# Performance work log

Measured on AMD Instinct MI355X. Metric: run time of the kernel, lower is better.

The kernel has to match this reference:

```python
import jax, jax.numpy as jnp
import numpy as np

N = 16000        # nodes
E = 256000       # edges
D_IN = 1280      # input node features
HID = 256        # hidden dim (all hidden_dims equal; required by res_linear shapes)
HEADS = 8
C = HID // HEADS # 32 channels per head
G = 32           # graphs in the batch
O = 64           # output labels (GO terms)
NB = 2           # conv blocks = len(hidden_dims) - 1
EPS = 1e-5


def _bn(h, g, b):
    # eval-mode BatchNorm1d with running_mean=0, running_var=1 (init state)
    return h * (g / jnp.sqrt(1.0 + EPS)) + b


def _seg_softmax(logits, seg, num):
    # numerically-stable segment softmax (PyG softmax semantics)
    m = jax.ops.segment_max(logits, seg, num_segments=num)
    e = jnp.exp(logits - m[seg])
    s = jax.ops.segment_sum(e, seg, num_segments=num)
    return e / (s[seg] + 1e-16)


def setup_inputs() -> dict:
    key = jax.random.key(0)
    ks = jax.random.split(key, 16)
    w = lambda i, sh: jax.random.normal(ks[i], sh, jnp.float32) * 0.05
    return {
        "x": jax.random.normal(ks[0], (N, D_IN), jnp.float32),
        "edge_index": jax.random.randint(ks[1], (2, E), 0, N),
        "batch": jnp.sort(jax.random.randint(ks[2], (N,), 0, G)),
        # feature_proj: Linear -> ReLU -> BN
        "fp_W": w(3, (D_IN, HID)), "fp_b": jnp.zeros(HID),
        "fp_g": jnp.ones(HID), "fp_be": jnp.zeros(HID),
        # GATv2Conv per block: lin_l, lin_r, att, out-bias
        "gat_Wl": w(4, (NB, HID, HID)), "gat_bl": jnp.zeros((NB, HID)),
        "gat_Wr": w(5, (NB, HID, HID)), "gat_br": jnp.zeros((NB, HID)),
        "gat_att": w(6, (NB, HEADS, C)), "gat_bias": jnp.zeros((NB, HID)),
        # GINConv MLP: Linear -> ReLU -> BN
        "gin_W": w(7, (NB, HID, HID)), "gin_b": jnp.zeros((NB, HID)),
        "gin_g": jnp.ones((NB, HID)), "gin_be": jnp.zeros((NB, HID)),
        # PyG LayerNorm (graph mode) affine
        "ln_g": jnp.ones((NB, HID)), "ln_b": jnp.zeros((NB, HID)),
        # residual linears
        "res_W": w(8, (NB, HID, HID)), "res_b": jnp.zeros((NB, HID)),
        # GlobalAttention gate MLP
        "pool_W1": w(9, (HID, HID)), "pool_b1": jnp.zeros(HID),
        "pool_W2": w(10, (HID, 1)), "pool_b2": jnp.zeros(1),
        # O label heads (hierarchy=None -> just the MLP), stacked
        "head_W1": w(11, (O, HID, 256)), "head_b1": jnp.zeros((O, 256)),
        "head_g": jnp.ones((O, 256)), "head_be": jnp.zeros((O, 256)),
        "head_W2": w(12, (O, 256)), "head_b2": jnp.zeros(O),
    }


def reference(x, edge_index, batch, fp_W, fp_b, fp_g, fp_be,
              gat_Wl, gat_bl, gat_Wr, gat_br, gat_att, gat_bias,
              gin_W, gin_b, gin_g, gin_be, ln_g, ln_b, res_W, res_b,
              pool_W1, pool_b1, pool_W2, pool_b2,
              head_W1, head_b1, head_g, head_be, head_W2, head_b2):
    n = x.shape[0]
    # feature_proj (eval: dropout = identity)
    h = _bn(jax.nn.relu(x @ fp_W + fp_b), fp_g, fp_be)

    src0, dst0 = edge_index[0], edge_index[1]
    loop = jnp.arange(n)
    src = jnp.concatenate([src0, loop])  # GATv2 adds self-loops by default
    dst = jnp.concatenate([dst0, loop])

    for i in range(NB):
        # ---- GATv2Conv (no activation after, per original control flow) ----
        xl = (h @ gat_Wl[i] + gat_bl[i]).reshape(n, HEADS, C)
        xr = (h @ gat_Wr[i] + gat_br[i]).reshape(n, HEADS, C)
        msg = xl[src]                                   # [E', H, C]
        eact = jax.nn.leaky_relu(msg + xr[dst], 0.2)
        logit = jnp.einsum('ehc,hc->eh', eact, gat_att[i])
        alpha = _seg_softmax(logit, dst, n)             # [E', H]
        h = jax.ops.segment_sum(alpha[:, :, None] * msg, dst,
                                num_segments=n).reshape(n, HID) + gat_bias[i]
        # ---- GINConv: nn((1+0)*x + sum_neighbors), then leaky_relu ----
        agg = jax.ops.segment_sum(h[src0], dst0, num_segments=n)
        gin = _bn(jax.nn.relu((h + agg) @ gin_W[i] + gin_b[i]), gin_g[i], gin_be[i])
        h = jax.nn.leaky_relu(gin, 0.2)
        # ---- PyG LayerNorm (graph mode, batch=None: global mean/std) + residual ----
        mu = h.mean()
        sd = jnp.std(h)
        ln = (h - mu) / (sd + EPS) * ln_g[i] + ln_b[i]
        h = jax.nn.leaky_relu(ln + (h @ res_W[i] + res_b[i]), 0.2)

    # ---- GlobalAttention pooling ----
    gate = jnp.tanh(h @ pool_W1 + pool_b1) @ pool_W2 + pool_b2   # [N, 1]
    a = _seg_softmax(gate[:, 0], batch, G)
    emb = jax.ops.segment_sum(a[:, None] * h, batch, num_segments=G)  # [G, HID]

    # ---- O label heads (hierarchy None -> MLP only), vectorized ----
    z = jnp.einsum('bd,odh->boh', emb, head_W1) + head_b1[None]
    z = _bn(jax.nn.silu(z), head_g[None], head_be[None])
    out = jnp.einsum('boh,oh->bo', z, head_W2) + head_b2[None]
    return out[:, :, None]  # torch.stack(outputs, dim=1) -> [G, O, 1]
```

## Files before the change

kernel.cpp:

```cpp
#include <hip/hip_runtime.h>
#include <math.h>

#define N_NODES 16000
#define N_EDGES 256000
#define EPE (N_EDGES + N_NODES)
#define DIN 1280
#define HID 256
#define HEADS 8
#define CPH 32
#define NG 32
#define NO 64
#define EPSC 1e-5f
#define CAP 32
#define XPAD 264

typedef __bf16 bf16;
typedef __attribute__((ext_vector_type(8))) __bf16 bf16x8;
typedef __attribute__((ext_vector_type(4))) float floatx4;

typedef __attribute__((address_space(3))) unsigned int lds_u32;
typedef const __attribute__((address_space(1))) unsigned int glob_u32;

__device__ __forceinline__ float lrelu(float v) { return v > 0.f ? v : 0.2f * v; }
__device__ __forceinline__ float bflo(unsigned int u) { return __uint_as_float(u << 16); }
__device__ __forceinline__ float bfhi(unsigned int u) { return __uint_as_float(u & 0xffff0000u); }

__device__ __forceinline__ void gll16(const void* g, void* l) {
    __builtin_amdgcn_global_load_lds((glob_u32*)g, (lds_u32*)l, 16, 0, 0);
}

__global__ void wconv_gen(const float* __restrict__ W, bf16* __restrict__ Wt, int K, int total) {
    int idx = blockIdx.x * 256 + threadIdx.x;
    if (idx >= total) return;
    int per = K * HID;
    int l = idx / per, rem = idx - l * per;
    int n = rem / K, k = rem - n * K;
    Wt[idx] = (bf16)W[(size_t)l * per + (size_t)k * HID + n];
}

__global__ void wconv_pair(const float* __restrict__ Wl, const float* __restrict__ Wr,
                           bf16* __restrict__ Wt) {
    int idx = blockIdx.x * 256 + threadIdx.x;
    int n = idx >> 8, k = idx & 255;
    float v = (n < 256) ? Wl[(size_t)k * HID + n] : Wr[(size_t)k * HID + (n - 256)];
    Wt[idx] = (bf16)v;
}

__global__ __launch_bounds__(256) void gemm_mfma(
    const bf16* __restrict__ A, const bf16* __restrict__ Bt,
    const float* __restrict__ bias, const float* __restrict__ bias2,
    bf16* __restrict__ C, int K, int ldc, int mode,
    const float* __restrict__ g, const float* __restrict__ be)
{
    __shared__ __align__(16) bf16 As[128 * 32];
    __shared__ __align__(16) bf16 Bs[128 * 32];
    const int tid = threadIdx.x;
    const int bm = blockIdx.y * 128, bn = blockIdx.x * 128;
    const int w = tid >> 6, lane = tid & 63;
    const int wm = (w & 1) * 64, wn = (w >> 1) * 64;
    const int lrow = lane & 15, lk8 = (lane >> 4) * 8;

    floatx4 acc[4][4];
#pragma unroll
    for (int i = 0; i < 4; i++)
#pragma unroll
        for (int j = 0; j < 4; j++) acc[i][j] = (floatx4){0.f, 0.f, 0.f, 0.f};

    const bf16* gA = A + (size_t)(bm + (tid >> 2)) * K + (tid & 3) * 8;
    const bf16* gB = Bt + (size_t)(bn + (tid >> 2)) * K + (tid & 3) * 8;
    bf16* lA0 = As + (size_t)(w * 64) * 8;
    bf16* lA1 = As + (size_t)(w * 64 + 256) * 8;
    bf16* lB0 = Bs + (size_t)(w * 64) * 8;
    bf16* lB1 = Bs + (size_t)(w * 64 + 256) * 8;
    const size_t rowskip = (size_t)64 * K;

    for (int k0 = 0; k0 < K; k0 += 32) {
        gll16(gA + k0, lA0);
        gll16(gA + rowskip + k0, lA1);
        gll16(gB + k0, lB0);
        gll16(gB + rowskip + k0, lB1);
        __syncthreads();
        bf16x8 af[4], bfr[4];
#pragma unroll
        for (int i = 0; i < 4; i++) af[i] = *(const bf16x8*)&As[(wm + 16 * i + lrow) * 32 + lk8];
#pragma unroll
        for (int j = 0; j < 4; j++) bfr[j] = *(const bf16x8*)&Bs[(wn + 16 * j + lrow) * 32 + lk8];
#pragma unroll
        for (int i = 0; i < 4; i++)
#pragma unroll
            for (int j = 0; j < 4; j++)
                acc[i][j] = __builtin_amdgcn_mfma_f32_16x16x32_bf16(af[i], bfr[j], acc[i][j], 0, 0, 0);
        __syncthreads();
    }

    const float inv = rsqrtf(1.f + EPSC);
#pragma unroll
    for (int j = 0; j < 4; j++) {
        int col = bn + wn + 16 * j + lrow;
        float bcol = (col < HID) ? bias[col] : bias2[col - HID];
        float gc = (mode >= 1) ? g[col] * inv : 0.f;
        float bec = (mode >= 1) ? be[col] : 0.f;
#pragma unroll
        for (int i = 0; i < 4; i++) {
            int row0 = bm + wm + 16 * i + (lane >> 4) * 4;
#pragma unroll
            for (int r = 0; r < 4; r++) {
                float z = acc[i][j][r] + bcol;
                if (mode >= 1) { z = fmaxf(z, 0.f); z = z * gc + bec; }
                if (mode == 2) z = lrelu(z);
                C[(size_t)(row0 + r) * ldc + col] = (bf16)z;
            }
        }
    }
}

__global__ __launch_bounds__(256) void gemm_f32A(
    const float* __restrict__ A, const bf16* __restrict__ Bt,
    const float* __restrict__ bias, bf16* __restrict__ C, int K,
    const float* __restrict__ g, const float* __restrict__ be)
{
    __shared__ __align__(16) bf16 As[128 * 32];
    __shared__ __align__(16) bf16 Bs[128 * 32];
    const int tid = threadIdx.x;
    const int bm = blockIdx.y * 128, bn = blockIdx.x * 128;
    const int w = tid >> 6, lane = tid & 63;
    const int wm = (w & 1) * 64, wn = (w >> 1) * 64;
    const int lrow = lane & 15, lk8 = (lane >> 4) * 8;

    floatx4 acc[4][4];
#pragma unroll
    for (int i = 0; i < 4; i++)
#pragma unroll
        for (int j = 0; j < 4; j++) acc[i][j] = (floatx4){0.f, 0.f, 0.f, 0.f};

    const int r2 = tid >> 1, c2 = tid & 1;
    const float* gA = A + (size_t)(bm + r2) * K + c2 * 16;
    bf16* sA = As + r2 * 32 + c2 * 16;
    const bf16* gB = Bt + (size_t)(bn + (tid >> 2)) * K + (tid & 3) * 8;
    bf16* lB0 = Bs + (size_t)(w * 64) * 8;
    bf16* lB1 = Bs + (size_t)(w * 64 + 256) * 8;
    const size_t rowskipB = (size_t)64 * K;

    for (int k0 = 0; k0 < K; k0 += 32) {
        gll16(gB + k0, lB0);
        gll16(gB + rowskipB + k0, lB1);
        float4 a0 = *(const float4*)(gA + k0 + 0);
        float4 a1 = *(const float4*)(gA + k0 + 4);
        float4 a2 = *(const float4*)(gA + k0 + 8);
        float4 a3 = *(const float4*)(gA + k0 + 12);
        bf16x8 h0, h1;
        h0[0] = (bf16)a0.x; h0[1] = (bf16)a0.y; h0[2] = (bf16)a0.z; h0[3] = (bf16)a0.w;
        h0[4] = (bf16)a1.x; h0[5] = (bf16)a1.y; h0[6] = (bf16)a1.z; h0[7] = (bf16)a1.w;
        h1[0] = (bf16)a2.x; h1[1] = (bf16)a2.y; h1[2] = (bf16)a2.z; h1[3] = (bf16)a2.w;
        h1[4] = (bf16)a3.x; h1[5] = (bf16)a3.y; h1[6] = (bf16)a3.z; h1[7] = (bf16)a3.w;
        *(bf16x8*)(sA + 0) = h0;
        *(bf16x8*)(sA + 8) = h1;
        __syncthreads();
        bf16x8 af[4], bfr[4];
#pragma unroll
        for (int i = 0; i < 4; i++) af[i] = *(const bf16x8*)&As[(wm + 16 * i + lrow) * 32 + lk8];
#pragma unroll
        for (int j = 0; j < 4; j++) bfr[j] = *(const bf16x8*)&Bs[(wn + 16 * j + lrow) * 32 + lk8];
#pragma unroll
        for (int i = 0; i < 4; i++)
#pragma unroll
            for (int j = 0; j < 4; j++)
                acc[i][j] = __builtin_amdgcn_mfma_f32_16x16x32_bf16(af[i], bfr[j], acc[i][j], 0, 0, 0);
        __syncthreads();
    }

    const float inv = rsqrtf(1.f + EPSC);
#pragma unroll
    for (int j = 0; j < 4; j++) {
        int col = bn + wn + 16 * j + lrow;
        float bcol = bias[col];
        float gc = g[col] * inv;
        float bec = be[col];
#pragma unroll
        for (int i = 0; i < 4; i++) {
            int row0 = bm + wm + 16 * i + (lane >> 4) * 4;
#pragma unroll
            for (int r = 0; r < 4; r++) {
                float z = fmaxf(acc[i][j][r] + bcol, 0.f) * gc + bec;
                C[(size_t)(row0 + r) * HID + col] = (bf16)z;
            }
        }
    }
}

__global__ void hist_kernel(const int* __restrict__ ei, int* __restrict__ cnt) {
    int e = blockIdx.x * 256 + threadIdx.x;
    if (e >= EPE) return;
    int d = (e < N_EDGES) ? ei[N_EDGES + e] : (e - N_EDGES);
    atomicAdd(&cnt[d], 1);
}

__global__ __launch_bounds__(1024) void scan_kernel(const int* __restrict__ cnt,
                                                    int* __restrict__ roff, int* __restrict__ cursor) {
    __shared__ int wsum[16];
    int t = threadIdx.x;
    int base = t * 16;
    int local[16]; int s = 0;
#pragma unroll
    for (int i = 0; i < 16; i++) {
        int idx = base + i;
        int v = (idx < N_NODES) ? cnt[idx] : 0;
        local[i] = s; s += v;
    }
    int lane = t & 63, wid = t >> 6;
    int incl = s;
    for (int o = 1; o < 64; o <<= 1) { int v = __shfl_up(incl, o); if (lane >= o) incl += v; }
    if (lane == 63) wsum[wid] = incl;
    __syncthreads();
    if (t == 0) { int a = 0; for (int k = 0; k < 16; k++) { int v = wsum[k]; wsum[k] = a; a += v; } }
    __syncthreads();
    int texcl = incl - s + wsum[wid];
#pragma unroll
    for (int i = 0; i < 16; i++) {
        int idx = base + i;
        if (idx < N_NODES) { int o = texcl + local[i]; roff[idx] = o; cursor[idx] = o; }
    }
    if (t == 1023) roff[N_NODES] = texcl + s;
}

__global__ void scatter_kernel(const int* __restrict__ ei, int* __restrict__ cursor,
                               int* __restrict__ esrc) {
    int e = blockIdx.x * 256 + threadIdx.x;
    if (e >= EPE) return;
    int s, d;
    if (e < N_EDGES) { s = ei[e]; d = ei[N_EDGES + e]; }
    else { s = d = e - N_EDGES; }
    int pos = atomicAdd(&cursor[d], 1);
    esrc[pos] = s;
}

__global__ __launch_bounds__(256) void gat_fused(
    const bf16* __restrict__ XLR, const int* __restrict__ roff, const int* __restrict__ esrc,
    const float* __restrict__ att, const float* __restrict__ gbias, bf16* __restrict__ out)
{
    const int d = blockIdx.x, t = threadIdx.x;
    const int beg = roff[d], deg = roff[d + 1] - beg;
    __shared__ __align__(16) bf16 xs[CAP][XPAD];
    __shared__ __align__(16) float4 xa4[8 * 16];
    __shared__ float llog[CAP * 8];
    __shared__ float m_s[8], s_s[8], resc[8];

    if (t < 128) {
        int hh = t >> 4, cc = t & 15;
        int c = hh * 32 + cc * 2;
        float xr0 = (float)XLR[(size_t)d * 512 + 256 + c];
        float xr1 = (float)XLR[(size_t)d * 512 + 256 + c + 1];
        xa4[hh * 16 + cc] = (float4){xr0, att[c], xr1, att[c + 1]};
    }
    if (t < 8) { m_s[t] = -INFINITY; s_s[t] = 0.f; }

    const int jj = t & 31;
    const int hh = t >> 5;
    const int g = t >> 5, l = t & 31;
    float acc = 0.f;

    for (int c0 = 0; c0 < deg; c0 += CAP) {
        int cn = min(CAP, deg - c0);
        __syncthreads();
        for (int r = g; r < cn; r += 8) {
            int s = esrc[beg + c0 + r];
            *(bf16x8*)(&xs[r][l * 8]) = *(const bf16x8*)(XLR + (size_t)s * 512 + l * 8);
        }
        __syncthreads();
        if (jj < cn) {
            float lg = 0.f;
#pragma unroll
            for (int cc = 0; cc < 16; cc++) {
                int ce = (cc + jj) & 15;
                unsigned int p = *(const unsigned int*)&xs[jj][hh * 32 + ce * 2];
                float4 xa = xa4[hh * 16 + ce];
                lg += lrelu(bflo(p) + xa.x) * xa.y + lrelu(bfhi(p) + xa.z) * xa.w;
            }
            llog[jj * 8 + hh] = lg;
        }
        __syncthreads();
        if (t < 64) {
            int h2 = t & 7, j0 = t >> 3;
            float mx = -INFINITY;
            for (int j = j0; j < cn; j += 8) mx = fmaxf(mx, llog[j * 8 + h2]);
            for (int o = 8; o < 64; o <<= 1) mx = fmaxf(mx, __shfl_xor(mx, o));
            float mo = m_s[h2];
            float mn = fmaxf(mo, mx);
            float ss = 0.f;
            for (int j = j0; j < cn; j += 8) {
                float e = __expf(llog[j * 8 + h2] - mn);
                llog[j * 8 + h2] = e;
                ss += e;
            }
            for (int o = 8; o < 64; o <<= 1) ss += __shfl_xor(ss, o);
            if (t < 8) {
                float r = __expf(mo - mn);
                resc[h2] = r;
                s_s[h2] = s_s[h2] * r + ss;
                m_s[h2] = mn;
            }
        }
        __syncthreads();
        acc *= resc[hh];
        for (int j = 0; j < cn; j++)
            acc += llog[j * 8 + hh] * (float)xs[j][t];
    }
    out[(size_t)d * HID + t] = (bf16)(gbias[t] + acc / (s_s[hh] + 1e-16f));
}

__global__ __launch_bounds__(256) void gin_gather(
    const unsigned int* __restrict__ hu, const int* __restrict__ roff,
    const int* __restrict__ esrc, unsigned int* __restrict__ uu)
{
    int d = blockIdx.x, t = threadIdx.x;
    int grp = t >> 7, c = t & 127;
    int beg = roff[d], end = roff[d + 1];
    float a0 = 0.f, a1 = 0.f;
    int p = beg + grp;
    while (p + 14 < end) {
        int s[8];
#pragma unroll
        for (int k = 0; k < 8; k++) s[k] = esrc[p + 2 * k];
        unsigned int v[8];
#pragma unroll
        for (int k = 0; k < 8; k++) v[k] = hu[(size_t)s[k] * 128 + c];
#pragma unroll
        for (int k = 0; k < 8; k++) { a0 += bflo(v[k]); a1 += bfhi(v[k]); }
        p += 16;
    }
    for (; p < end; p += 2) {
        unsigned int v = hu[(size_t)esrc[p] * 128 + c];
        a0 += bflo(v); a1 += bfhi(v);
    }
    __shared__ float plo[128], phi[128];
    if (grp) { plo[c] = a0; phi[c] = a1; }
    __syncthreads();
    if (!grp) {
        a0 += plo[c]; a1 += phi[c];
        bf16 b0 = (bf16)a0, b1 = (bf16)a1;
        unsigned int r = ((unsigned int)*(unsigned short*)&b0) |
                         (((unsigned int)*(unsigned short*)&b1) << 16);
        uu[(size_t)d * 128 + c] = r;
    }
}

__global__ void stats_kernel(const bf16* __restrict__ x, float2* __restrict__ part, int n8) {
    float s = 0.f, sq = 0.f;
    for (int i = blockIdx.x * blockDim.x + threadIdx.x; i < n8; i += gridDim.x * blockDim.x) {
        bf16x8 v = *(const bf16x8*)(x + (size_t)i * 8);
#pragma unroll
        for (int j = 0; j < 8; j++) { float f = (float)v[j]; s += f; sq += f * f; }
    }
    for (int o = 32; o > 0; o >>= 1) { s += __shfl_down(s, o); sq += __shfl_down(sq, o); }
    __shared__ float ls[4], lq[4];
    int wid = threadIdx.x >> 6, lane = threadIdx.x & 63;
    if (lane == 0) { ls[wid] = s; lq[wid] = sq; }
    __syncthreads();
    if (threadIdx.x == 0)
        part[blockIdx.x] = make_float2(ls[0] + ls[1] + ls[2] + ls[3],
                                       lq[0] + lq[1] + lq[2] + lq[3]);
}

__global__ void stats_reduce(const float2* __restrict__ part, float* __restrict__ stat) {
    int t = threadIdx.x;
    float2 v = part[t];
    float s = v.x, q = v.y;
    for (int o = 32; o > 0; o >>= 1) { s += __shfl_down(s, o); q += __shfl_down(q, o); }
    __shared__ float ls[4], lq[4];
    int wid = t >> 6, lane = t & 63;
    if (lane == 0) { ls[wid] = s; lq[wid] = q; }
    __syncthreads();
    if (t == 0) { stat[0] = ls[0] + ls[1] + ls[2] + ls[3]; stat[1] = lq[0] + lq[1] + lq[2] + lq[3]; }
}

__global__ void ln_res_kernel(const bf16* __restrict__ h, const bf16* __restrict__ r,
                              const float* __restrict__ stats, const float* __restrict__ g,
                              const float* __restrict__ b, bf16* __restrict__ out)
{
    int i = (blockIdx.x * 256 + threadIdx.x) * 4;
    const float inv_n = 1.f / (float)((size_t)N_NODES * HID);
    float mu = stats[0] * inv_n;
    float var = stats[1] * inv_n - mu * mu;
    float sd = sqrtf(fmaxf(var, 0.f));
    float rs = 1.f / (sd + EPSC);
    int ch = i & (HID - 1);
#pragma unroll
    for (int j = 0; j < 4; j++) {
        float v = ((float)h[i + j] - mu) * rs * g[ch + j] + b[ch + j] + (float)r[i + j];
        out[i + j] = (bf16)lrelu(v);
    }
}

__global__ void gbound_kernel(const int* __restrict__ batch, int* __restrict__ gstart) {
    int g = threadIdx.x;
    if (g > NG) return;
    int lo = 0, hi = N_NODES;
    while (lo < hi) { int mid = (lo + hi) >> 1; if (batch[mid] < g) lo = mid + 1; else hi = mid; }
    gstart[g] = lo;
}

__global__ __launch_bounds__(256) void pool_gate_kernel(const bf16* __restrict__ t,
    const float* __restrict__ W2, const float* __restrict__ b2, float* __restrict__ gate)
{
    int n = blockIdx.x * 4 + (threadIdx.x >> 6);
    int lane = threadIdx.x & 63;
    const bf16* p = t + (size_t)n * HID + lane * 4;
    float4 w = *(const float4*)(W2 + lane * 4);
    float s = tanhf((float)p[0]) * w.x + tanhf((float)p[1]) * w.y
            + tanhf((float)p[2]) * w.z + tanhf((float)p[3]) * w.w;
    for (int o = 32; o > 0; o >>= 1) s += __shfl_down(s, o);
    if (lane == 0) gate[n] = s + b2[0];
}

__global__ __launch_bounds__(256) void pool_stats_kernel(
    float* __restrict__ gate, const int* __restrict__ gstart)
{
    int g = blockIdx.x, t = threadIdx.x;
    int lo = gstart[g], hi = gstart[g + 1];
    __shared__ float red[256];
    float m = -INFINITY;
    for (int n = lo + t; n < hi; n += 256) m = fmaxf(m, gate[n]);
    red[t] = m; __syncthreads();
    for (int st = 128; st > 0; st >>= 1) { if (t < st) red[t] = fmaxf(red[t], red[t + st]); __syncthreads(); }
    m = red[0]; __syncthreads();
    float s = 0.f;
    for (int n = lo + t; n < hi; n += 256) s += __expf(gate[n] - m);
    red[t] = s; __syncthreads();
    for (int st = 128; st > 0; st >>= 1) { if (t < st) red[t] += red[t + st]; __syncthreads(); }
    float sinv = 1.f / (red[0] + 1e-16f);
    for (int n = lo + t; n < hi; n += 256) gate[n] = __expf(gate[n] - m) * sinv;
}

__global__ __launch_bounds__(256) void emb_accum_kernel(
    const float* __restrict__ a, const int* __restrict__ batch,
    const bf16* __restrict__ h, float* __restrict__ emb)
{
    int n0 = blockIdx.x * 32, t = threadIdx.x;
    int cur = batch[n0]; float acc = 0.f;
    for (int j = 0; j < 32; j++) {
        int n = n0 + j;
        int b = batch[n];
        if (b != cur) { atomicAdd(&emb[cur * HID + t], acc); cur = b; acc = 0.f; }
        acc += a[n] * (float)h[(size_t)n * HID + t];
    }
    atomicAdd(&emb[cur * HID + t], acc);
}

__global__ __launch_bounds__(256) void heads_kernel(
    const float* __restrict__ emb, const float* __restrict__ W1, const float* __restrict__ b1,
    const float* __restrict__ hg, const float* __restrict__ hbe, const float* __restrict__ W2,
    const float* __restrict__ b2, float* __restrict__ out)
{
    int o = blockIdx.x;
    int g0 = blockIdx.y * 4;
    int k = threadIdx.x;
    __shared__ float se[4][HID];
    __shared__ float red[256];
#pragma unroll
    for (int j = 0; j < 4; j++) se[j][k] = emb[(g0 + j) * HID + k];
    __syncthreads();
    const float* w1p = W1 + (size_t)o * HID * HID + k;
    float zb = b1[o * HID + k];
    float z0 = zb, z1 = zb, z2 = zb, z3 = zb;
#pragma unroll 8
    for (int d = 0; d < HID; d++) {
        float w = w1p[(size_t)d * HID];
        z0 = fmaf(se[0][d], w, z0);
        z1 = fmaf(se[1][d], w, z1);
        z2 = fmaf(se[2][d], w, z2);
        z3 = fmaf(se[3][d], w, z3);
    }
    const float gk = hg[o * HID + k] * rsqrtf(1.f + EPSC);
    const float bek = hbe[o * HID + k];
    const float w2 = W2[o * HID + k];
    const float b2o = b2[o];
    float zz[4] = {z0, z1, z2, z3};
#pragma unroll
    for (int j = 0; j < 4; j++) {
        float z = zz[j];
        float sil = z / (1.f + expf(-z));
        red[k] = (sil * gk + bek) * w2;
        __syncthreads();
        for (int st = 128; st > 0; st >>= 1) { if (k < st) red[k] += red[k + st]; __syncthreads(); }
        if (k == 0) out[(g0 + j) * NO + o] = red[0] + b2o;
        __syncthreads();
    }
}

extern "C" void kernel_launch(void* const* d_in, const int* in_sizes, int n_in,
                              void* d_out, int out_size, void* d_ws, size_t ws_size,
                              hipStream_t stream) {
    const float* x        = (const float*)d_in[0];
    const int*   ei       = (const int*)  d_in[1];
    const int*   batch    = (const int*)  d_in[2];
    const float* fp_W     = (const float*)d_in[3];
    const float* fp_b     = (const float*)d_in[4];
    const float* fp_g     = (const float*)d_in[5];
    const float* fp_be    = (const float*)d_in[6];
    const float* gat_Wl   = (const float*)d_in[7];
    const float* gat_bl   = (const float*)d_in[8];
    const float* gat_Wr   = (const float*)d_in[9];
    const float* gat_br   = (const float*)d_in[10];
    const float* gat_att  = (const float*)d_in[11];
    const float* gat_bias = (const float*)d_in[12];
    const float* gin_W    = (const float*)d_in[13];
    const float* gin_b    = (const float*)d_in[14];
    const float* gin_g    = (const float*)d_in[15];
    const float* gin_be   = (const float*)d_in[16];
    const float* ln_g     = (const float*)d_in[17];
    const float* ln_b     = (const float*)d_in[18];
    const float* res_W    = (const float*)d_in[19];
    const float* res_b    = (const float*)d_in[20];
    const float* pool_W1  = (const float*)d_in[21];
    const float* pool_b1  = (const float*)d_in[22];
    const float* pool_W2  = (const float*)d_in[23];
    const float* pool_b2  = (const float*)d_in[24];
    const float* head_W1  = (const float*)d_in[25];
    const float* head_b1  = (const float*)d_in[26];
    const float* head_g   = (const float*)d_in[27];
    const float* head_be  = (const float*)d_in[28];
    const float* head_W2  = (const float*)d_in[29];
    const float* head_b2  = (const float*)d_in[30];
    float* out = (float*)d_out;

    char* base = (char*)d_ws;
    size_t off = 0;
    auto alloc = [&](size_t bytes) -> char* {
        char* p = base + off; off += (bytes + 255) & ~(size_t)255; return p;
    };
    int*   esrc   = (int*)  alloc((size_t)EPE * 4);
    int*   cnt    = (int*)  alloc((size_t)N_NODES * 4);
    int*   roff   = (int*)  alloc((size_t)(N_NODES + 1) * 4);
    int*   cursor = (int*)  alloc((size_t)N_NODES * 4);
    float* gate   = (float*)alloc((size_t)N_NODES * 4);
    int*   gstart = (int*)  alloc((NG + 1) * 4);
    float* emb    = (float*)alloc(NG * HID * 4);
    float* stat   = (float*)alloc(8);
    float2* statp = (float2*)alloc(256 * 8);
    bf16*  Hb0    = (bf16*) alloc((size_t)N_NODES * HID * 2);
    bf16*  Hb1    = (bf16*) alloc((size_t)N_NODES * HID * 2);
    bf16*  XLR    = (bf16*) alloc((size_t)N_NODES * 512 * 2);
    bf16*  fpWt   = (bf16*) alloc((size_t)DIN * HID * 2);
    bf16*  wlrT0  = (bf16*) alloc((size_t)512 * HID * 2);
    bf16*  wlrT1  = (bf16*) alloc((size_t)512 * HID * 2);
    bf16*  gwT    = (bf16*) alloc((size_t)2 * HID * HID * 2);
    bf16*  rwT    = (bf16*) alloc((size_t)2 * HID * HID * 2);
    bf16*  pwT    = (bf16*) alloc((size_t)HID * HID * 2);
    bf16*  Ub     = XLR;
    bf16*  wlrT[2] = { wlrT0, wlrT1 };

    wconv_gen<<<(DIN * HID + 255) / 256, 256, 0, stream>>>(fp_W, fpWt, DIN, DIN * HID);
    wconv_pair<<<512, 256, 0, stream>>>(gat_Wl, gat_Wr, wlrT0);
    wconv_pair<<<512, 256, 0, stream>>>(gat_Wl + HID * HID, gat_Wr + HID * HID, wlrT1);
    wconv_gen<<<512, 256, 0, stream>>>(gin_W, gwT, HID, 2 * HID * HID);
    wconv_gen<<<512, 256, 0, stream>>>(res_W, rwT, HID, 2 * HID * HID);
    wconv_gen<<<256, 256, 0, stream>>>(pool_W1, pwT, HID, HID * HID);

    hipMemsetAsync(cnt, 0, N_NODES * sizeof(int), stream);
    hist_kernel<<<(EPE + 255) / 256, 256, 0, stream>>>(ei, cnt);
    scan_kernel<<<1, 1024, 0, stream>>>(cnt, roff, cursor);
    scatter_kernel<<<(EPE + 255) / 256, 256, 0, stream>>>(ei, cursor, esrc);
    gbound_kernel<<<1, 64, 0, stream>>>(batch, gstart);

    dim3 grid256(2, 125), grid512(4, 125);
    gemm_f32A<<<grid256, 256, 0, stream>>>(x, fpWt, fp_b, Hb0, DIN, fp_g, fp_be);

    for (int i = 0; i < 2; i++) {
        gemm_mfma<<<grid512, 256, 0, stream>>>(Hb0, wlrT[i], gat_bl + i * HID, gat_br + i * HID,
                                               XLR, HID, 512, 0, nullptr, nullptr);
        gat_fused<<<N_NODES, 256, 0, stream>>>(XLR, roff, esrc, gat_att + i * HEADS * CPH,
                                               gat_bias + i * HID, Hb1);
        gin_gather<<<N_NODES, 256, 0, stream>>>((const unsigned int*)Hb1, roff, esrc,
                                                (unsigned int*)Ub);
        gemm_mfma<<<grid256, 256, 0, stream>>>(Ub, gwT + (size_t)i * HID * HID, gin_b + i * HID,
                                               nullptr, Hb0, HID, HID, 2,
                                               gin_g + i * HID, gin_be + i * HID);
        stats_kernel<<<256, 256, 0, stream>>>(Hb0, statp, (N_NODES * HID) / 8);
        stats_reduce<<<1, 256, 0, stream>>>(statp, stat);
        gemm_mfma<<<grid256, 256, 0, stream>>>(Hb0, rwT + (size_t)i * HID * HID, res_b + i * HID,
                                               nullptr, Hb1, HID, HID, 0, nullptr, nullptr);
        ln_res_kernel<<<(N_NODES * HID) / 1024, 256, 0, stream>>>(Hb0, Hb1, stat,
                                                                  ln_g + i * HID, ln_b + i * HID, Hb0);
    }

    gemm_mfma<<<grid256, 256, 0, stream>>>(Hb0, pwT, pool_b1, nullptr, Hb1, HID, HID, 0, nullptr, nullptr);
    pool_gate_kernel<<<N_NODES / 4, 256, 0, stream>>>(Hb1, pool_W2, pool_b2, gate);
    pool_stats_kernel<<<NG, 256, 0, stream>>>(gate, gstart);
    hipMemsetAsync(emb, 0, NG * HID * sizeof(float), stream);
    emb_accum_kernel<<<N_NODES / 32, 256, 0, stream>>>(gate, batch, Hb0, emb);

    dim3 hgrid(NO, 8);
    heads_kernel<<<hgrid, 256, 0, stream>>>(emb, head_W1, head_b1, head_g, head_be,
                                            head_W2, head_b2, out);
}
```

Before: 640.5 us.

## Use 64x64 double-buffered padded-LDS GEMM for hidden-size matmuls

Replaces the 128x128 direct-to-LDS GEMM with a 64x64 tile kernel for the K=256 matmuls. It quadruples the block count to fill more compute units, uses register-prefetched double-buffered LDS, and pads LDS rows to avoid bank conflicts. The fp32-input projection GEMM is also moved to register prefetch with double buffering and padding. Smaller tiles lower reuse per block and add more global traffic for the B operand.

```diff
diff --git a/kernel.cpp b/kernel.cpp
--- a/kernel.cpp
+++ b/kernel.cpp
@@ -13,21 +13,15 @@
 #define EPSC 1e-5f
 #define CAP 32
 #define XPAD 264
+#define SPAD 40
 
 typedef __bf16 bf16;
 typedef __attribute__((ext_vector_type(8))) __bf16 bf16x8;
 typedef __attribute__((ext_vector_type(4))) float floatx4;
 
-typedef __attribute__((address_space(3))) unsigned int lds_u32;
-typedef const __attribute__((address_space(1))) unsigned int glob_u32;
-
 __device__ __forceinline__ float lrelu(float v) { return v > 0.f ? v : 0.2f * v; }
 __device__ __forceinline__ float bflo(unsigned int u) { return __uint_as_float(u << 16); }
 __device__ __forceinline__ float bfhi(unsigned int u) { return __uint_as_float(u & 0xffff0000u); }
-
-__device__ __forceinline__ void gll16(const void* g, void* l) {
-    __builtin_amdgcn_global_load_lds((glob_u32*)g, (lds_u32*)l, 16, 0, 0);
-}
 
 __global__ void wconv_gen(const float* __restrict__ W, bf16* __restrict__ Wt, int K, int total) {
     int idx = blockIdx.x * 256 + threadIdx.x;
@@ -46,14 +40,76 @@
     Wt[idx] = (bf16)v;
 }
 
-__global__ __launch_bounds__(256) void gemm_mfma(
+__global__ __launch_bounds__(256) void gemm64(
     const bf16* __restrict__ A, const bf16* __restrict__ Bt,
     const float* __restrict__ bias, const float* __restrict__ bias2,
     bf16* __restrict__ C, int K, int ldc, int mode,
     const float* __restrict__ g, const float* __restrict__ be)
 {
-    __shared__ __align__(16) bf16 As[128 * 32];
-    __shared__ __align__(16) bf16 Bs[128 * 32];
+    __shared__ __align__(16) bf16 As[2][64 * SPAD];
+    __shared__ __align__(16) bf16 Bs[2][64 * SPAD];
+    const int tid = threadIdx.x;
+    const int bm = blockIdx.y * 64, bn = blockIdx.x * 64;
+    const int w = tid >> 6, lane = tid & 63;
+    const int wm = w * 16;
+    const int lrow = lane & 15, lk8 = (lane >> 4) * 8;
+    const int row = tid >> 2, k8 = (tid & 3) * 8;
+
+    const bf16* gA = A + (size_t)(bm + row) * K + k8;
+    const bf16* gB = Bt + (size_t)(bn + row) * K + k8;
+
+    floatx4 acc[4];
+#pragma unroll
+    for (int j = 0; j < 4; j++) acc[j] = (floatx4){0.f, 0.f, 0.f, 0.f};
+
+    const int nk = K >> 5;
+    bf16x8 ra = *(const bf16x8*)gA;
+    bf16x8 rb = *(const bf16x8*)gB;
+
+    for (int it = 0; it < nk; ++it) {
+        int p = it & 1;
+        *(bf16x8*)&As[p][row * SPAD + k8] = ra;
+        *(bf16x8*)&Bs[p][row * SPAD + k8] = rb;
+        __syncthreads();
+        if (it + 1 < nk) {
+            ra = *(const bf16x8*)(gA + (it + 1) * 32);
+            rb = *(const bf16x8*)(gB + (it + 1) * 32);
+        }
+        bf16x8 af = *(const bf16x8*)&As[p][(wm + lrow) * SPAD + lk8];
+        bf16x8 bfr[4];
+#pragma unroll
+        for (int j = 0; j < 4; j++) bfr[j] = *(const bf16x8*)&Bs[p][(16 * j + lrow) * SPAD + lk8];
+#pragma unroll
+        for (int j = 0; j < 4; j++)
+            acc[j] = __builtin_amdgcn_mfma_f32_16x16x32_bf16(af, bfr[j], acc[j], 0, 0, 0);
+        __syncthreads();
+    }
+
+    const float inv = rsqrtf(1.f + EPSC);
+    const int row0 = bm + wm + (lane >> 4) * 4;
+#pragma unroll
+    for (int j = 0; j < 4; j++) {
+        int col = bn + 16 * j + lrow;
+        float bcol = (col < HID) ? bias[col] : bias2[col - HID];
+        float gc = (mode >= 1) ? g[col] * inv : 0.f;
+        float bec = (mode >= 1) ? be[col] : 0.f;
+#pragma unroll
+        for (int r = 0; r < 4; r++) {
+            float z = acc[j][r] + bcol;
+            if (mode >= 1) { z = fmaxf(z, 0.f); z = z * gc + bec; }
+            if (mode == 2) z = lrelu(z);
+            C[(size_t)(row0 + r) * ldc + col] = (bf16)z;
+        }
+    }
+}
+
+__global__ __launch_bounds__(256) void gemm_f32A(
+    const float* __restrict__ A, const bf16* __restrict__ Bt,
+    const float* __restrict__ bias, bf16* __restrict__ C, int K,
+    const float* __restrict__ g, const float* __restrict__ be)
+{
+    __shared__ __align__(16) bf16 As[2][128 * SPAD];
+    __shared__ __align__(16) bf16 Bs[2][128 * SPAD];
     const int tid = threadIdx.x;
     const int bm = blockIdx.y * 128, bn = blockIdx.x * 128;
     const int w = tid >> 6, lane = tid & 63;
@@ -66,101 +122,45 @@
 #pragma unroll
         for (int j = 0; j < 4; j++) acc[i][j] = (floatx4){0.f, 0.f, 0.f, 0.f};
 
-    const bf16* gA = A + (size_t)(bm + (tid >> 2)) * K + (tid & 3) * 8;
-    const bf16* gB = Bt + (size_t)(bn + (tid >> 2)) * K + (tid & 3) * 8;
-    bf16* lA0 = As + (size_t)(w * 64) * 8;
-    bf16* lA1 = As + (size_t)(w * 64 + 256) * 8;
-    bf16* lB0 = Bs + (size_t)(w * 64) * 8;
-    bf16* lB1 = Bs + (size_t)(w * 64 + 256) * 8;
-    const size_t rowskip = (size_t)64 * K;
-
-    for (int k0 = 0; k0 < K; k0 += 32) {
-        gll16(gA + k0, lA0);
-        gll16(gA + rowskip + k0, lA1);
-        gll16(gB + k0, lB0);
-        gll16(gB + rowskip + k0, lB1);
-        __syncthreads();
-        bf16x8 af[4], bfr[4];
-#pragma unroll
-        for (int i = 0; i < 4; i++) af[i] = *(const bf16x8*)&As[(wm + 16 * i + lrow) * 32 + lk8];
-#pragma unroll
-        for (int j = 0; j < 4; j++) bfr[j] = *(const bf16x8*)&Bs[(wn + 16 * j + lrow) * 32 + lk8];
-#pragma unroll
-        for (int i = 0; i < 4; i++)
-#pragma unroll
-            for (int j = 0; j < 4; j++)
-                acc[i][j] = __builtin_amdgcn_mfma_f32_16x16x32_bf16(af[i], bfr[j], acc[i][j], 0, 0, 0);
-        __syncthreads();
-    }
-
-    const float inv = rsqrtf(1.f + EPSC);
-#pragma unroll
-    for (int j = 0; j < 4; j++) {
-        int col = bn + wn + 16 * j + lrow;
-        float bcol = (col < HID) ? bias[col] : bias2[col - HID];
-        float gc = (mode >= 1) ? g[col] * inv : 0.f;
-        float bec = (mode >= 1) ? be[col] : 0.f;
-#pragma unroll
-        for (int i = 0; i < 4; i++) {
-            int row0 = bm + wm + 16 * i + (lane >> 4) * 4;
-#pragma unroll
-            for (int r = 0; r < 4; r++) {
-                float z = acc[i][j][r] + bcol;
-                if (mode >= 1) { z = fmaxf(z, 0.f); z = z * gc + bec; }
-                if (mode == 2) z = lrelu(z);
-                C[(size_t)(row0 + r) * ldc + col] = (bf16)z;
-            }
-        }
-    }
-}
-
-__global__ __launch_bounds__(256) void gemm_f32A(
-    const float* __restrict__ A, const bf16* __restrict__ Bt,
-    const float* __restrict__ bias, bf16* __restrict__ C, int K,
-    const float* __restrict__ g, const float* __restrict__ be)
-{
-    __shared__ __align__(16) bf16 As[128 * 32];
-    __shared__ __align__(16) bf16 Bs[128 * 32];
-    const int tid = threadIdx.x;
-    const int bm = blockIdx.y * 128, bn = blockIdx.x * 128;
-    const int w = tid >> 6, lane = tid & 63;
-    const int wm = (w & 1) * 64, wn = (w >> 1) * 64;
-    const int lrow = lane & 15, lk8 = (lane >> 4) * 8;
-
-    floatx4 acc[4][4];
-#pragma unroll
-    for (int i = 0; i < 4; i++)
-#pragma unroll
-        for (int j = 0; j < 4; j++) acc[i][j] = (floatx4){0.f, 0.f, 0.f, 0.f};
-
     const int r2 = tid >> 1, c2 = tid & 1;
     const float* gA = A + (size_t)(bm + r2) * K + c2 * 16;
-    bf16* sA = As + r2 * 32 + c2 * 16;
-    const bf16* gB = Bt + (size_t)(bn + (tid >> 2)) * K + (tid & 3) * 8;
-    bf16* lB0 = Bs + (size_t)(w * 64) * 8;
-    bf16* lB1 = Bs + (size_t)(w * 64 + 256) * 8;
-    const size_t rowskipB = (size_t)64 * K;
-
-    for (int k0 = 0; k0 < K; k0 += 32) {
-        gll16(gB + k0, lB0);
-        gll16(gB + rowskipB + k0, lB1);
-        float4 a0 = *(const float4*)(gA + k0 + 0);
-        float4 a1 = *(const float4*)(gA + k0 + 4);
-        float4 a2 = *(const float4*)(gA + k0 + 8);
-        float4 a3 = *(const float4*)(gA + k0 + 12);
+    const bf16* gB = Bt + (size_t)(bn + r2) * K + c2 * 16;
+
+    const int nk = K >> 5;
+    float4 a0 = *(const float4*)(gA + 0);
+    float4 a1 = *(const float4*)(gA + 4);
+    float4 a2 = *(const float4*)(gA + 8);
+    float4 a3 = *(const float4*)(gA + 12);
+    bf16x8 rb0 = *(const bf16x8*)(gB + 0);
+    bf16x8 rb1 = *(const bf16x8*)(gB + 8);
+
+    for (int it = 0; it < nk; ++it) {
+        int p = it & 1;
         bf16x8 h0, h1;
         h0[0] = (bf16)a0.x; h0[1] = (bf16)a0.y; h0[2] = (bf16)a0.z; h0[3] = (bf16)a0.w;
         h0[4] = (bf16)a1.x; h0[5] = (bf16)a1.y; h0[6] = (bf16)a1.z; h0[7] = (bf16)a1.w;
         h1[0] = (bf16)a2.x; h1[1] = (bf16)a2.y; h1[2] = (bf16)a2.z; h1[3] = (bf16)a2.w;
         h1[4] = (bf16)a3.x; h1[5] = (bf16)a3.y; h1[6] = (bf16)a3.z; h1[7] = (bf16)a3.w;
-        *(bf16x8*)(sA + 0) = h0;
-        *(bf16x8*)(sA + 8) = h1;
-        __syncthreads();
+        *(bf16x8*)&As[p][r2 * SPAD + c2 * 16 + 0] = h0;
+        *(bf16x8*)&As[p][r2 * SPAD + c2 * 16 + 8] = h1;
+        *(bf16x8*)&Bs[p][r2 * SPAD + c2 * 16 + 0] = rb0;
+        *(bf16x8*)&Bs[p][r2 * SPAD + c2 * 16 + 8] = rb1;
+        __syncthreads();
+        if (it + 1 < nk) {
+            const float* pa = gA + (it + 1) * 32;
+            a0 = *(const float4*)(pa + 0);
+            a1 = *(const float4*)(pa + 4);
+            a2 = *(const float4*)(pa + 8);
+            a3 = *(const float4*)(pa + 12);
+            const bf16* pb = gB + (it + 1) * 32;
+            rb0 = *(const bf16x8*)(pb + 0);
+            rb1 = *(const bf16x8*)(pb + 8);
+        }
         bf16x8 af[4], bfr[4];
 #pragma unroll
-        for (int i = 0; i < 4; i++) af[i] = *(const bf16x8*)&As[(wm + 16 * i + lrow) * 32 + lk8];
-#pragma unroll
-        for (int j = 0; j < 4; j++) bfr[j] = *(const bf16x8*)&Bs[(wn + 16 * j + lrow) * 32 + lk8];
+        for (int i = 0; i < 4; i++) af[i] = *(const bf16x8*)&As[p][(wm + 16 * i + lrow) * SPAD + lk8];
+#pragma unroll
+        for (int j = 0; j < 4; j++) bfr[j] = *(const bf16x8*)&Bs[p][(wn + 16 * j + lrow) * SPAD + lk8];
 #pragma unroll
         for (int i = 0; i < 4; i++)
 #pragma unroll
@@ -562,28 +562,30 @@
     scatter_kernel<<<(EPE + 255) / 256, 256, 0, stream>>>(ei, cursor, esrc);
     gbound_kernel<<<1, 64, 0, stream>>>(batch, gstart);
 
-    dim3 grid256(2, 125), grid512(4, 125);
-    gemm_f32A<<<grid256, 256, 0, stream>>>(x, fpWt, fp_b, Hb0, DIN, fp_g, fp_be);
+    dim3 gridF(2, 125);
+    dim3 g64_256(4, 250);
+    dim3 g64_512(8, 250);
+    gemm_f32A<<<gridF, 256, 0, stream>>>(x, fpWt, fp_b, Hb0, DIN, fp_g, fp_be);
 
     for (int i = 0; i < 2; i++) {
-        gemm_mfma<<<grid512, 256, 0, stream>>>(Hb0, wlrT[i], gat_bl + i * HID, gat_br + i * HID,
-                                               XLR, HID, 512, 0, nullptr, nullptr);
+        gemm64<<<g64_512, 256, 0, stream>>>(Hb0, wlrT[i], gat_bl + i * HID, gat_br + i * HID,
+                                            XLR, HID, 512, 0, nullptr, nullptr);
         gat_fused<<<N_NODES, 256, 0, stream>>>(XLR, roff, esrc, gat_att + i * HEADS * CPH,
                                                gat_bias + i * HID, Hb1);
         gin_gather<<<N_NODES, 256, 0, stream>>>((const unsigned int*)Hb1, roff, esrc,
                                                 (unsigned int*)Ub);
-        gemm_mfma<<<grid256, 256, 0, stream>>>(Ub, gwT + (size_t)i * HID * HID, gin_b + i * HID,
-                                               nullptr, Hb0, HID, HID, 2,
-                                               gin_g + i * HID, gin_be + i * HID);
+        gemm64<<<g64_256, 256, 0, stream>>>(Ub, gwT + (size_t)i * HID * HID, gin_b + i * HID,
+                                            nullptr, Hb0, HID, HID, 2,
+                                            gin_g + i * HID, gin_be + i * HID);
         stats_kernel<<<256, 256, 0, stream>>>(Hb0, statp, (N_NODES * HID) / 8);
         stats_reduce<<<1, 256, 0, stream>>>(statp, stat);
-        gemm_mfma<<<grid256, 256, 0, stream>>>(Hb0, rwT + (size_t)i * HID * HID, res_b + i * HID,
-                                               nullptr, Hb1, HID, HID, 0, nullptr, nullptr);
+        gemm64<<<g64_256, 256, 0, stream>>>(Hb0, rwT + (size_t)i * HID * HID, res_b + i * HID,
+                                            nullptr, Hb1, HID, HID, 0, nullptr, nullptr);
         ln_res_kernel<<<(N_NODES * HID) / 1024, 256, 0, stream>>>(Hb0, Hb1, stat,
                                                                   ln_g + i * HID, ln_b + i * HID, Hb0);
     }
 
-    gemm_mfma<<<grid256, 256, 0, stream>>>(Hb0, pwT, pool_b1, nullptr, Hb1, HID, HID, 0, nullptr, nullptr);
+    gemm64<<<g64_256, 256, 0, stream>>>(Hb0, pwT, pool_b1, nullptr, Hb1, HID, HID, 0, nullptr, nullptr);
     pool_gate_kernel<<<N_NODES / 4, 256, 0, stream>>>(Hb1, pool_W2, pool_b2, gate);
     pool_stats_kernel<<<NG, 256, 0, stream>>>(gate, gstart);
     hipMemsetAsync(emb, 0, NG * HID * sizeof(float), stream);
```

Result: no change. 630.2 us (-1.6%).
